# Performance work log

Measured on AMD Instinct MI355X. Metric: run time of the kernel, lower is better.

The kernel has to match this reference:

```python
import jax, jax.numpy as jnp
import numpy as np

ANCHORS = np.array([[4.63,1.97,1.74],[6.93,2.51,2.84],[6.37,2.85,3.19],[10.5,2.94,3.47],
                    [12.29,2.9,3.87],[0.5,2.53,0.98],[2.11,0.77,1.47],[1.7,0.6,1.28],
                    [0.73,0.67,1.77],[0.41,0.41,1.07]], dtype=np.float32)  # [10,3] nuScenes anchor sizes
BINS = 20          # anchor_size_bins
TEXT_DIM = 3 * BINS
NUM_PROPOSALS = 200
NMS_K = 3


def _vector_values():
    la = np.log(ANCHORS)
    return np.linspace(la.min() - 0.1, la.max() - 0.1, BINS).astype(np.float32)


def _anchor_vecs_normed():
    # soft_relu_bin_vectors: soft-bin log-anchors into BINS bins per dim, dim-major flatten
    vals = _vector_values()
    inc = vals[1] - vals[0]
    la = np.log(ANCHORS)                                      # [10,3]
    v = np.clip((la[:, :, None] - vals[None, None, :]) / inc, 0.0, 1.0)  # [10,3,BINS]
    v = v.reshape(10, TEXT_DIM)
    return (v / (1e-8 + np.linalg.norm(v, axis=1, keepdims=True))).astype(np.float32)


def conv2d(x, w, b=None):
    y = jax.lax.conv_general_dilated(x, w, (1, 1), 'SAME',
                                     dimension_numbers=('NCHW', 'OIHW', 'NCHW'))
    if b is not None:
        y = y + b[None, :, None, None]
    return y


def iou_sim_vec(a):
    # vectorized form of the triple-nested loop: prod over dims of min/max ratio
    mn = jnp.minimum(a[:, None, :], a[None, :, :])
    mx = jnp.maximum(a[:, None, :], a[None, :, :])
    return jnp.prod(mn / mx, axis=-1)                         # [10,10]


def setup_inputs() -> dict:
    key = jax.random.key(0)
    ks = jax.random.split(key, 8)
    B, Cin, hid, H, W = 2, 512, 128, 180, 180
    feats = jax.random.normal(ks[0], (B, Cin, H, W), jnp.float32)
    w_shared = jax.random.normal(ks[1], (hid, Cin, 3, 3), jnp.float32) * 0.02
    b_shared = jnp.zeros((hid,), jnp.float32)
    w_bb = jax.random.normal(ks[2], (hid, hid, 3, 3), jnp.float32) * 0.05
    gamma_bb = jnp.ones((hid,), jnp.float32)
    beta_bb = jnp.zeros((hid,), jnp.float32)
    w_hm = jax.random.normal(ks[3], (TEXT_DIM, hid, 3, 3), jnp.float32) * 0.05
    b_hm = jnp.zeros((TEXT_DIM,), jnp.float32)
    thr_scale = jnp.ones((1,), jnp.float32)                   # Threshold2d scale
    logit_scale = jnp.ones((1,), jnp.float32) * np.log(1.0 / 0.07)
    logit_bias = jnp.ones((1,), jnp.float32) * (-10.0)
    w_enc = jax.random.normal(ks[4], (hid, 3), jnp.float32) * 0.1  # Conv1d(3->hid, k=1)
    anchor_vecs = jnp.asarray(_anchor_vecs_normed())
    xs = jnp.arange(W, dtype=jnp.float32) + 0.5
    ys = jnp.arange(H, dtype=jnp.float32) + 0.5
    gy, gx = jnp.meshgrid(ys, xs, indexing='ij')
    bev_pos = jnp.stack([gx.reshape(-1), gy.reshape(-1)], axis=-1)  # [H*W, 2]
    return dict(feats=feats, w_shared=w_shared, b_shared=b_shared, w_bb=w_bb,
                gamma_bb=gamma_bb, beta_bb=beta_bb, w_hm=w_hm, b_hm=b_hm,
                thr_scale=thr_scale, logit_scale=logit_scale, logit_bias=logit_bias,
                w_enc=w_enc, anchor_vecs=anchor_vecs, bev_pos=bev_pos)


def reference(feats, w_shared, b_shared, w_bb, gamma_bb, beta_bb, w_hm, b_hm,
              thr_scale, logit_scale, logit_bias, w_enc, anchor_vecs, bev_pos):
    B, _, H, W = feats.shape
    # shared conv
    lidar_feat = conv2d(feats, w_shared, b_shared)            # [B,hid,H,W]
    # BasicBlock2D: conv + (inference) BN + ReLU
    x = conv2d(lidar_feat, w_bb)
    x = jax.nn.relu(x * gamma_bb[None, :, None, None] + beta_bb[None, :, None, None])
    # heatmap conv -> Threshold2d (sigmoid((x - thresholds) * scale))
    vec = conv2d(x, w_hm, b_hm)                               # [B,60,H,W]
    thresholds = jnp.asarray(np.tile(_vector_values(), 3))[None, :, None, None]
    vec = jax.nn.sigmoid((vec - thresholds) * thr_scale[0])
    # cosine sim vs normalized anchor bin-vectors -> per-class heatmap
    vecn = vec / (1e-8 + jnp.linalg.norm(vec, axis=1, keepdims=True))
    sim = jnp.einsum('bchw,kc->bkhw', vecn, anchor_vecs)      # [B,10,H,W]
    heatmap = jax.nn.sigmoid(logit_scale[0] * sim + logit_bias[0])
    # NMS: keep only local maxima within nms_kernel_size window
    local_max = jax.lax.reduce_window(heatmap, -jnp.inf, jax.lax.max,
                                      (1, 1, NMS_K, NMS_K), (1, 1, 1, 1), 'SAME')
    hm_nms = jnp.where(heatmap == local_max, heatmap, 0.0)
    # top-k proposals over classes x positions
    flat = hm_nms.reshape(B, -1)                              # [B, 10*H*W]
    top_scores, top_idx = jax.lax.top_k(flat, NUM_PROPOSALS)
    top_labels = top_idx // (H * W)                           # [B,P]
    top_pos = top_idx % (H * W)                               # [B,P]
    # gather proposal features, heatmap scores and bev positions
    hid = lidar_feat.shape[1]
    lidar_flat = lidar_feat.reshape(B, hid, H * W)
    idx_f = jnp.broadcast_to(top_pos[:, None, :], (B, hid, NUM_PROPOSALS))
    query_feat = jnp.take_along_axis(lidar_flat, idx_f, axis=2)  # [B,hid,P]
    hm_flat = heatmap.reshape(B, 10, H * W)
    idx_h = jnp.broadcast_to(top_pos[:, None, :], (B, 10, NUM_PROPOSALS))
    query_hm_score = jnp.take_along_axis(hm_flat, idx_h, axis=2)  # [B,10,P]
    query_pos = bev_pos[top_pos]                              # [B,P,2]
    # anchor value encoding (Conv1d(3->hid,k=1) on log-anchor sizes of top classes)
    top_anchor = jnp.log(jnp.asarray(ANCHORS))[top_labels]    # [B,P,3]
    query_feat = query_feat + jnp.einsum('cd,bpd->bcp', w_enc, top_anchor)
    sims = iou_sim_vec(jnp.asarray(ANCHORS))                  # [10,10] anchor IoU similarity
    return heatmap, top_scores, top_labels, query_feat, query_pos, query_hm_score, sims
```

## Files before the change

kernel.cpp:

```cpp
#include <hip/hip_runtime.h>
#include <math.h>


#define HW 180
#define NPIX 32400
#define NCLS 10
#define NPROP 200
#define HID 128
#define TDIM 60
#define NBIG (NCLS*NPIX)

#define TH_LO  (-0.9915981193)
#define TH_STEP (0.1789675812)

__constant__ float c_anchors[10][3] = {
  {4.63f,1.97f,1.74f},{6.93f,2.51f,2.84f},{6.37f,2.85f,3.19f},{10.5f,2.94f,3.47f},
  {12.29f,2.9f,3.87f},{0.5f,2.53f,0.98f},{2.11f,0.77f,1.47f},{1.7f,0.6f,1.28f},
  {0.73f,0.67f,1.77f},{0.41f,0.41f,1.07f}};

using f16x8 = _Float16 __attribute__((ext_vector_type(8)));
using f16x4 = _Float16 __attribute__((ext_vector_type(4)));
using f32x4 = float    __attribute__((ext_vector_type(4)));

#define GLD_LDS16(g, l) __builtin_amdgcn_global_load_lds( \
    (__attribute__((address_space(1))) void*)(g), \
    (__attribute__((address_space(3))) void*)(l), 16, 0, 0)

__device__ __forceinline__ void w_tr(const float* __restrict__ w, _Float16* __restrict__ dst,
                                     int CIN, int KS, int HALVES, int cout, int i) {
  int N = HALVES * KS * 36864;
  if (i >= N) return;
  int j = i & 7;
  int lane = (i >> 3) & 63;
  int mf = (i >> 9) & 3;
  int rest = i >> 11;
  int tsl = rest % 9; rest /= 9;
  int t = (tsl % 3) * 3 + (tsl / 3);
  int plane = rest & 1; rest >>= 1;
  int ks = rest % KS; int h = rest / KS;
  int co = h * 64 + mf * 16 + (lane & 15);
  int ch = ks * 32 + (lane >> 4) * 8 + j;
  float v = (co < cout) ? w[((size_t)co * CIN + ch) * 9 + t] : 0.f;
  _Float16 hi = (_Float16)v;
  dst[i] = plane ? (_Float16)(v - (float)hi) : hi;
}

__global__ __launch_bounds__(256)
void prep_kernel(const float* __restrict__ w_shared, const float* __restrict__ w_bb,
                 const float* __restrict__ w_hm, const float* __restrict__ feats,
                 _Float16* __restrict__ W1, _Float16* __restrict__ W2,
                 _Float16* __restrict__ W3, _Float16* __restrict__ X1,
                 float* __restrict__ out_sims, int* __restrict__ cnt) {
  int bid = blockIdx.x;
  const int tid = threadIdx.x;
  if (bid < 4608) { w_tr(w_shared, W1, 512, 16, 2, 128, bid * 256 + tid); return; }
  bid -= 4608;
  if (bid < 1152) { w_tr(w_bb, W2, 128, 4, 2, 128, bid * 256 + tid); return; }
  bid -= 1152;
  if (bid < 576)  { w_tr(w_hm, W3, 128, 4, 1, 60, bid * 256 + tid); return; }
  bid -= 576;
  if (bid < 4064) {
    int px = (bid % 127) * 256 + tid;
    int bks = bid / 127; int b = bks >> 4; int ks = bks & 15;
    if (px >= NPIX) return;
    const float* src = feats + ((size_t)(b * 512 + ks * 32)) * NPIX + px;
    float v[32];
#pragma unroll
    for (int c = 0; c < 32; ++c) v[c] = src[(size_t)c * NPIX];
    f16x8 hv[4], lv[4];
#pragma unroll
    for (int c = 0; c < 32; ++c) {
      _Float16 h = (_Float16)v[c];
      hv[c >> 3][c & 7] = h;
      lv[c >> 3][c & 7] = (_Float16)(v[c] - (float)h);
    }
    size_t ob = ((size_t)(b * 16 + ks) * NPIX + px) * 32;
#pragma unroll
    for (int i = 0; i < 4; ++i) {
      *(f16x8*)(X1 + ob + i * 8) = hv[i];
      *(f16x8*)(X1 + 33177600u + ob + i * 8) = lv[i];
    }
    return;
  }
  if (tid < 100) {
    int i = tid / 10, j = tid % 10;
    float r = 1.f;
#pragma unroll
    for (int d = 0; d < 3; ++d) {
      float ai = c_anchors[i][d], aj = c_anchors[j][d];
      r *= fminf(ai, aj) / fmaxf(ai, aj);
    }
    out_sims[tid] = r;
  }
  if (tid == 128) { cnt[0] = 0; cnt[1] = 0; }
}

template<int KS, int EPI>
__global__ __launch_bounds__(256, 2)
void conv_mfma(const _Float16* __restrict__ X, const _Float16* __restrict__ W,
               const float* __restrict__ p0, const float* __restrict__ p1,
               float* __restrict__ out0, _Float16* __restrict__ outX,
               const float* __restrict__ thr_scale, const float* __restrict__ logit_scale,
               const float* __restrict__ logit_bias, const float* __restrict__ anchor_vecs) {
  constexpr unsigned XPS = 2u * KS * NPIX * 32;
  constexpr bool DBUF = (EPI != 2);
  extern __shared__ _Float16 dlds[];
  _Float16* lds_x = dlds;
  _Float16* wA = dlds + 16128;
  _Float16* wB = dlds + 28416;
  float* lds_av = (float*)(dlds + 28416);

  const int x0 = blockIdx.x * 16;
  const int y0 = blockIdx.y * 12;
  const int b  = (EPI == 2) ? blockIdx.z : (blockIdx.z >> 1);
  const int h  = (EPI == 2) ? 0 : (blockIdx.z & 1);
  const int tid = threadIdx.x;
  const int wave = tid >> 6;
  const int lane = tid & 63;
  const int xl = lane & 15, kg = lane >> 4;

  {
    unsigned* p = (unsigned*)lds_x;
    for (int i = tid; i < 8064; i += 256) p[i] = 0u;
    if (EPI == 2)
      for (int i = tid; i < 600; i += 256) lds_av[i] = anchor_vecs[i];
  }

  unsigned offs[8]; unsigned okb = 0;
#pragma unroll
  for (int s = 0; s < 8; ++s) {
    int inst = wave + 4 * s;
    int c = inst * 64 + lane;
    bool valid = (c < 2016);
    int plane = (c >= 1008) ? 1 : 0;
    int cc = c - plane * 1008;
    int px = cc >> 2, q = cc & 3;
    int r = px / 18, xx = px - r * 18;
    int gy = y0 - 1 + r, gx = x0 - 1 + xx;
    bool ok = valid && ((unsigned)gy < 180u) && ((unsigned)gx < 180u);
    offs[s] = ok ? ((unsigned)((b * KS) * NPIX + gy * 180 + gx) * 32u + (unsigned)q * 8u
                    + (unsigned)plane * XPS) : 0u;
    okb |= (ok ? 1u : 0u) << s;
  }

  f32x4 acc[4][3];
#pragma unroll
  for (int mf = 0; mf < 4; ++mf)
#pragma unroll
    for (int f = 0; f < 3; ++f) acc[mf][f] = (f32x4){0.f, 0.f, 0.f, 0.f};

  auto COMPUTE = [&](int g, const _Float16* wbuf) {
    f16x8 bfh[5], bfl[5];
#pragma unroll
    for (int rr = 0; rr < 5; ++rr) {
      int lo = ((3 * wave + rr) * 18 + xl + g) * 32 + kg * 8;
      bfh[rr] = *(const f16x8*)(lds_x + lo);
      bfl[rr] = *(const f16x8*)(lds_x + 8064 + lo);
    }
#pragma unroll
    for (int ky = 0; ky < 3; ++ky) {
      const _Float16* wt = wbuf + ky * 2048 + lane * 8;
      f16x8 ah[4], al[4];
#pragma unroll
      for (int mf = 0; mf < 4; ++mf) {
        ah[mf] = *(const f16x8*)(wt + mf * 512);
        al[mf] = *(const f16x8*)(wt + 6144 + mf * 512);
      }
#pragma unroll
      for (int mf = 0; mf < 4; ++mf)
#pragma unroll
        for (int f = 0; f < 3; ++f) {
          acc[mf][f] = __builtin_amdgcn_mfma_f32_16x16x32_f16(ah[mf], bfh[f + ky], acc[mf][f], 0, 0, 0);
          acc[mf][f] = __builtin_amdgcn_mfma_f32_16x16x32_f16(ah[mf], bfl[f + ky], acc[mf][f], 0, 0, 0);
          acc[mf][f] = __builtin_amdgcn_mfma_f32_16x16x32_f16(al[mf], bfh[f + ky], acc[mf][f], 0, 0, 0);
        }
    }
  };
  auto WDMA = [&](const _Float16* gw, int g, _Float16* wbuf) {
#pragma unroll
    for (int s = 0; s < 6; ++s) {
      int c2 = wave + 4 * s;
      int pl = c2 / 12, idx = c2 - pl * 12;
      GLD_LDS16(gw + pl * 18432 + g * 6144 + idx * 512 + lane * 8,
                wbuf + pl * 6144 + idx * 512);
    }
  };
  auto XDMA = [&](unsigned kof) {
#pragma unroll
    for (int s = 0; s < 8; ++s) {
      if (okb & (1u << s))
        GLD_LDS16(X + (size_t)(offs[s] + kof), lds_x + (wave + 4 * s) * 512);
    }
  };

  const _Float16* gwb = W + (size_t)(h * KS) * 36864;
  for (int ks = 0; ks < KS; ++ks) {
    const unsigned kof = (unsigned)ks * (NPIX * 32u);
    const _Float16* gw = gwb + (size_t)ks * 36864;
    if (DBUF) {
      __syncthreads();
      XDMA(kof);
      WDMA(gw, 0, wA);
      __syncthreads();
      WDMA(gw, 1, wB);
      COMPUTE(0, wA);
      __syncthreads();
      WDMA(gw, 2, wA);
      COMPUTE(1, wB);
      __syncthreads();
      COMPUTE(2, wA);
    } else {
#pragma unroll
      for (int g = 0; g < 3; ++g) {
        __syncthreads();
        if (g == 0) XDMA(kof);
        WDMA(gw, g, wA);
        __syncthreads();
        COMPUTE(g, wA);
      }
    }
  }

  const int x = x0 + xl;
  if (EPI != 2) {
    if (x >= HW) return;
#pragma unroll
    for (int mf = 0; mf < 4; ++mf) {
      const int cobase = h * 64 + mf * 16 + kg * 4;
      f32x4 q0 = *(const f32x4*)(p0 + cobase);
      f32x4 q1 = (EPI == 1) ? *(const f32x4*)(p1 + cobase) : (f32x4){0.f,0.f,0.f,0.f};
#pragma unroll
      for (int f = 0; f < 3; ++f) {
        const int y = y0 + 3 * wave + f;
        const int kso = cobase >> 5, c32 = cobase & 31;
        size_t nidx = ((size_t)(b * 4 + kso) * NPIX + (size_t)y * 180 + x) * 32 + c32;
        if (EPI == 0) {
          f32x4 v;
          f16x4 h4, l4;
#pragma unroll
          for (int r = 0; r < 4; ++r) {
            float z = acc[mf][f][r] + q0[r];
            v[r] = z;
            _Float16 hh = (_Float16)z;
            h4[r] = hh;
            l4[r] = (_Float16)(z - (float)hh);
          }
          *(f32x4*)(out0 + nidx) = v;
          *(f16x4*)(outX + nidx) = h4;
          *(f16x4*)(outX + 8294400u + nidx) = l4;
        } else {
          f16x4 h4, l4;
#pragma unroll
          for (int r = 0; r < 4; ++r) {
            float z = fmaf(acc[mf][f][r], q0[r], q1[r]);
            z = fmaxf(z, 0.f);
            _Float16 hh = (_Float16)z;
            h4[r] = hh;
            l4[r] = (_Float16)(z - (float)hh);
          }
          *(f16x4*)(outX + nidx) = h4;
          *(f16x4*)(outX + 8294400u + nidx) = l4;
        }
      }
    }
  } else {
    const float s  = thr_scale[0];
    const float ls = logit_scale[0];
    const float lb = logit_bias[0];
    float bh4[4][4], th4[4][4];
    bool vmask[4];
#pragma unroll
    for (int mf = 0; mf < 4; ++mf) {
      const int cb = mf * 16 + kg * 4;
      vmask[mf] = (cb < TDIM);
#pragma unroll
      for (int r = 0; r < 4; ++r) {
        bh4[mf][r] = vmask[mf] ? p0[cb + r] : 0.f;
        th4[mf][r] = (float)(TH_LO + (double)((cb + r) % 20) * TH_STEP);
      }
    }
#pragma unroll
    for (int f = 0; f < 3; ++f) {
      const int y = y0 + 3 * wave + f;
      float v[4][4];
      float s2 = 0.f;
#pragma unroll
      for (int mf = 0; mf < 4; ++mf)
#pragma unroll
        for (int r = 0; r < 4; ++r) {
          float z = acc[mf][f][r] + bh4[mf][r];
          float t = (z - th4[mf][r]) * s;
          float vv = vmask[mf] ? 1.f / (1.f + expf(-t)) : 0.f;
          v[mf][r] = vv;
          s2 = fmaf(vv, vv, s2);
        }
      s2 += __shfl_xor(s2, 16);
      s2 += __shfl_xor(s2, 32);
      const float rs = 1.f / (1e-8f + sqrtf(s2));
      float hm[10];
#pragma unroll
      for (int k = 0; k < 10; ++k) {
        float d = 0.f;
#pragma unroll
        for (int mf = 0; mf < 4; ++mf) {
          const int cb = mf * 16 + kg * 4;
          f32x4 a = vmask[mf] ? *(const f32x4*)(lds_av + k * TDIM + cb)
                              : (f32x4){0.f, 0.f, 0.f, 0.f};
#pragma unroll
          for (int r = 0; r < 4; ++r) d = fmaf(v[mf][r], a[r], d);
        }
        d += __shfl_xor(d, 16);
        d += __shfl_xor(d, 32);
        hm[k] = 1.f / (1.f + expf(-fmaf(ls, d * rs, lb)));
      }
      if (x < HW) {
#pragma unroll
        for (int j = 0; j < 3; ++j) {
          int k = kg + 4 * j;
          if (k < NCLS)
            out0[((size_t)(b * NCLS + k) * HW + y) * HW + x] = hm[k];
        }
      }
    }
  }
}

__global__ __launch_bounds__(256)
void nms_kernel(const float* __restrict__ hm, float* __restrict__ ckey,
                int* __restrict__ cidx, int* __restrict__ cnt) {
  __shared__ int lcnt[2];
  __shared__ int lbase[2];
  const int tid = threadIdx.x;
  if (tid < 2) lcnt[tid] = 0;
  __syncthreads();

  int i = blockIdx.x * 256 + tid;
  bool surv = false; float v = 0.f; int bk = 0, p = 0;
  if (i < 2 * NBIG) {
    int x = i % HW; int y = (i / HW) % HW; int plane = i / NPIX;
    v = hm[i];
    float m = v;
#pragma unroll
    for (int dy = -1; dy <= 1; ++dy)
#pragma unroll
      for (int dx = -1; dx <= 1; ++dx) {
        int yy = y + dy, xx = x + dx;
        if ((unsigned)yy < (unsigned)HW && (unsigned)xx < (unsigned)HW)
          m = fmaxf(m, hm[((size_t)plane * NPIX) + yy * HW + xx]);
      }
    if (v == m) {
      surv = true;
      bk = i / NBIG;
      p = atomicAdd(&lcnt[bk], 1);
    }
  }
  __syncthreads();
  if (tid < 2 && lcnt[tid] > 0)
    lbase[tid] = atomicAdd(&cnt[tid], lcnt[tid]);
  __syncthreads();
  if (surv) {
    int slot = lbase[bk] + p;
    ckey[(size_t)bk * NBIG + slot] = v;
    cidx[(size_t)bk * NBIG + slot] = i - bk * NBIG;
  }
}

__global__ __launch_bounds__(1024)
void topk_kernel(const float* __restrict__ ckey, const int* __restrict__ cidx,
                 const int* __restrict__ cnt, const float* __restrict__ heatmap,
                 const float* __restrict__ bev_pos, float* __restrict__ out,
                 int* __restrict__ iws) {
  const int b = blockIdx.x;
  const int tid = threadIdx.x;
  const float* keys = ckey + (size_t)b * NBIG;
  const int* idxs = cidx + (size_t)b * NBIG;

  __shared__ unsigned hist[256];
  __shared__ unsigned sh_prefix;
  __shared__ int sh_want, sh_n;
  __shared__ int cntGT, cntTie;
  __shared__ unsigned gt_key[256], gt_idx[256];
  __shared__ unsigned tie_idx[2048];

  if (tid == 0) sh_n = cnt[b];
  __syncthreads();
  const int n = sh_n;

  unsigned prefix = 0; int want = NPROP;
  for (int shift = 24; shift >= 0; shift -= 8) {
    if (tid < 256) hist[tid] = 0u;
    __syncthreads();
    for (int i = tid; i < n; i += 1024) {
      unsigned k = __float_as_uint(keys[i]);
      bool match = (shift == 24) || ((k >> (shift + 8)) == (prefix >> (shift + 8)));
      if (match) atomicAdd(&hist[(k >> shift) & 255], 1u);
    }
    __syncthreads();
    if (tid == 0) {
      int cum = 0; int bsel = 0; sh_want = want;
      for (int bin = 255; bin >= 0; --bin) {
        cum += (int)hist[bin];
        if (cum >= want) { bsel = bin; sh_want = want - (cum - (int)hist[bin]); break; }
      }
      sh_prefix = prefix | ((unsigned)bsel << shift);
      cntGT = 0; cntTie = 0;
    }
    __syncthreads();
    prefix = sh_prefix; want = sh_want;
    __syncthreads();
  }
  const unsigned T = prefix;

  for (int i = tid; i < n; i += 1024) {
    unsigned k = __float_as_uint(keys[i]);
    if (k > T) {
      int p = atomicAdd(&cntGT, 1);
      if (p < 256) { gt_key[p] = k; gt_idx[p] = (unsigned)idxs[i]; }
    } else if (k == T) {
      int p = atomicAdd(&cntTie, 1);
      if (p < 2048) tie_idx[p] = (unsigned)idxs[i];
    }
  }
  __syncthreads();
  const int nGT = min(cntGT, 256);
  const int nTie = min(cntTie, 2048);

  for (int i = tid; i < 256; i += 1024)
    if (i >= nGT) { gt_key[i] = 0u; gt_idx[i] = 0xFFFFFFFFu; }
  for (int i = tid; i < 2048; i += 1024)
    if (i >= nTie) tie_idx[i] = 0xFFFFFFFFu;
  __syncthreads();

  for (int k2 = 2; k2 <= 256; k2 <<= 1) {
    for (int j = k2 >> 1; j > 0; j >>= 1) {
      for (int i = tid; i < 256; i += 1024) {
        int ixj = i ^ j;
        if (ixj > i) {
          unsigned ka = gt_key[i], kb = gt_key[ixj];
          unsigned ia = gt_idx[i], ib = gt_idx[ixj];
          bool firstA = (ka > kb) || (ka == kb && ia < ib);
          bool up = ((i & k2) == 0);
          if (up ? !firstA : firstA) {
            gt_key[i] = kb; gt_key[ixj] = ka;
            gt_idx[i] = ib; gt_idx[ixj] = ia;
          }
        }
      }
      __syncthreads();
    }
  }
  for (int k2 = 2; k2 <= 2048; k2 <<= 1) {
    for (int j = k2 >> 1; j > 0; j >>= 1) {
      for (int i = tid; i < 2048; i += 1024) {
        int ixj = i ^ j;
        if (ixj > i) {
          unsigned ia = tie_idx[i], ib = tie_idx[ixj];
          bool firstA = ia < ib;
          bool up = ((i & k2) == 0);
          if (up ? !firstA : firstA) { tie_idx[i] = ib; tie_idx[ixj] = ia; }
        }
      }
      __syncthreads();
    }
  }

  for (int r = tid; r < NPROP; r += 1024) {
    unsigned idx; float score;
    if (r < nGT) { idx = gt_idx[r]; score = __uint_as_float(gt_key[r]); }
    else         { idx = tie_idx[r - nGT]; score = __uint_as_float(T); }
    int label = (int)(idx / NPIX);
    int pos = (int)(idx - (unsigned)label * NPIX);
    out[648000 + b * NPROP + r] = score;
    out[648400 + b * NPROP + r] = (float)label;
    out[700000 + (b * NPROP + r) * 2 + 0] = bev_pos[pos * 2 + 0];
    out[700000 + (b * NPROP + r) * 2 + 1] = bev_pos[pos * 2 + 1];
#pragma unroll
    for (int k = 0; k < NCLS; ++k)
      out[700800 + (b * NCLS + k) * NPROP + r] = heatmap[(size_t)(b * NCLS + k) * NPIX + pos];
    iws[b * NPROP + r] = pos;
    iws[2 * NPROP + b * NPROP + r] = label;
  }
}

__global__ void gather_qf_kernel(const float* __restrict__ lidar, const float* __restrict__ w_enc,
                                 const int* __restrict__ iws, float* __restrict__ out_qf) {
  int p = blockIdx.x % NPROP;
  int b = blockIdx.x / NPROP;
  int c = threadIdx.x;
  int pos = iws[b * NPROP + p];
  int label = iws[2 * NPROP + b * NPROP + p];
  float la0 = logf(c_anchors[label][0]);
  float la1 = logf(c_anchors[label][1]);
  float la2 = logf(c_anchors[label][2]);
  float dot = w_enc[c * 3 + 0] * la0 + w_enc[c * 3 + 1] * la1 + w_enc[c * 3 + 2] * la2;
  float g = lidar[((size_t)(b * 4 + (c >> 5)) * NPIX + pos) * 32 + (c & 31)];
  out_qf[((size_t)b * HID + c) * NPROP + p] = g + dot;
}

extern "C" void kernel_launch(void* const* d_in, const int* in_sizes, int n_in,
                              void* d_out, int out_size, void* d_ws, size_t ws_size,
                              hipStream_t stream) {
  (void)in_sizes; (void)n_in; (void)out_size; (void)ws_size;
  const float* feats       = (const float*)d_in[0];
  const float* w_shared    = (const float*)d_in[1];
  const float* b_shared    = (const float*)d_in[2];
  const float* w_bb        = (const float*)d_in[3];
  const float* gamma_bb    = (const float*)d_in[4];
  const float* beta_bb     = (const float*)d_in[5];
  const float* w_hm        = (const float*)d_in[6];
  const float* b_hm        = (const float*)d_in[7];
  const float* thr_scale   = (const float*)d_in[8];
  const float* logit_scale = (const float*)d_in[9];
  const float* logit_bias  = (const float*)d_in[10];
  const float* w_enc       = (const float*)d_in[11];
  const float* anchor_vecs = (const float*)d_in[12];
  const float* bev_pos     = (const float*)d_in[13];
  float* out = (float*)d_out;

  float* ws = (float*)d_ws;
  size_t off = 0;
  _Float16* X1 = (_Float16*)(ws + off); off += 33177600;
  _Float16* X2 = (_Float16*)(ws + off); off += 8294400;
  float* lidarN = ws + off; off += 8294400;
  _Float16* X3 = (_Float16*)(ws + off); off += 8294400;
  _Float16* W1 = (_Float16*)(ws + off); off += 589824;
  _Float16* W2 = (_Float16*)(ws + off); off += 147456;
  _Float16* W3 = (_Float16*)(ws + off); off += 73728;
  float* ckey  = ws + off; off += (size_t)2 * NBIG;
  int*   cidx  = (int*)(ws + off); off += (size_t)2 * NBIG;
  int*   iws   = (int*)(ws + off); off += 800;
  int*   cnt   = (int*)(ws + off);

  prep_kernel<<<10401, 256, 0, stream>>>(w_shared, w_bb, w_hm, feats,
                                         W1, W2, W3, X1, out + 704800, cnt);

  const unsigned CONV_LDS = 81408;
  const unsigned HEAD_LDS = 59232;
  dim3 cgrid(12, 15, 4);
  conv_mfma<16,0><<<cgrid, 256, CONV_LDS, stream>>>(X1, W1, b_shared, nullptr, lidarN, X2,
                                                    nullptr, nullptr, nullptr, nullptr);
  conv_mfma<4, 1><<<cgrid, 256, CONV_LDS, stream>>>(X2, W2, gamma_bb, beta_bb, nullptr, X3,
                                                    nullptr, nullptr, nullptr, nullptr);
  dim3 hgrid(12, 15, 2);
  conv_mfma<4, 2><<<hgrid, 256, HEAD_LDS, stream>>>(X3, W3, b_hm, nullptr, out, nullptr,
                                                    thr_scale, logit_scale, logit_bias,
                                                    anchor_vecs);

  nms_kernel<<<(2*NBIG + 255)/256, 256, 0, stream>>>(out, ckey, cidx, cnt);
  topk_kernel<<<2, 1024, 0, stream>>>(ckey, cidx, cnt, out, bev_pos, out, iws);
  gather_qf_kernel<<<2*NPROP, 128, 0, stream>>>(lidarN, w_enc, iws, out + 648800);
}
```

Baseline: 519.8 us.

## Shrink conv LDS footprint by splitting weight planes and dropping double buffering

The conv kernel no longer double-buffers the hi/lo weight planes. It now loads the high weight plane into a single smaller LDS buffer, runs its MFMAs, then reloads the low plane into the same buffer for the remaining MFMA term. This cuts LDS per block and raises launch bounds to 3 waves-per-SIMD occupancy so more blocks can overlap. The cost is extra barriers per group and the loss of the overlap between weight DMA and compute.

```diff
diff --git a/kernel.cpp b/kernel.cpp
--- a/kernel.cpp
+++ b/kernel.cpp
@@ -96,19 +96,17 @@
 }
 
 template<int KS, int EPI>
-__global__ __launch_bounds__(256, 2)
+__global__ __launch_bounds__(256, 3)
 void conv_mfma(const _Float16* __restrict__ X, const _Float16* __restrict__ W,
                const float* __restrict__ p0, const float* __restrict__ p1,
                float* __restrict__ out0, _Float16* __restrict__ outX,
                const float* __restrict__ thr_scale, const float* __restrict__ logit_scale,
                const float* __restrict__ logit_bias, const float* __restrict__ anchor_vecs) {
   constexpr unsigned XPS = 2u * KS * NPIX * 32;
-  constexpr bool DBUF = (EPI != 2);
   extern __shared__ _Float16 dlds[];
   _Float16* lds_x = dlds;
-  _Float16* wA = dlds + 16128;
-  _Float16* wB = dlds + 28416;
-  float* lds_av = (float*)(dlds + 28416);
+  _Float16* lds_w = dlds + 16128;
+  float* lds_av = (float*)(dlds + 22272);
 
   const int x0 = blockIdx.x * 16;
   const int y0 = blockIdx.y * 12;
@@ -149,74 +147,67 @@
 #pragma unroll
     for (int f = 0; f < 3; ++f) acc[mf][f] = (f32x4){0.f, 0.f, 0.f, 0.f};
 
-  auto COMPUTE = [&](int g, const _Float16* wbuf) {
-    f16x8 bfh[5], bfl[5];
-#pragma unroll
-    for (int rr = 0; rr < 5; ++rr) {
-      int lo = ((3 * wave + rr) * 18 + xl + g) * 32 + kg * 8;
-      bfh[rr] = *(const f16x8*)(lds_x + lo);
-      bfl[rr] = *(const f16x8*)(lds_x + 8064 + lo);
-    }
-#pragma unroll
-    for (int ky = 0; ky < 3; ++ky) {
-      const _Float16* wt = wbuf + ky * 2048 + lane * 8;
-      f16x8 ah[4], al[4];
-#pragma unroll
-      for (int mf = 0; mf < 4; ++mf) {
-        ah[mf] = *(const f16x8*)(wt + mf * 512);
-        al[mf] = *(const f16x8*)(wt + 6144 + mf * 512);
-      }
-#pragma unroll
-      for (int mf = 0; mf < 4; ++mf)
-#pragma unroll
-        for (int f = 0; f < 3; ++f) {
-          acc[mf][f] = __builtin_amdgcn_mfma_f32_16x16x32_f16(ah[mf], bfh[f + ky], acc[mf][f], 0, 0, 0);
-          acc[mf][f] = __builtin_amdgcn_mfma_f32_16x16x32_f16(ah[mf], bfl[f + ky], acc[mf][f], 0, 0, 0);
-          acc[mf][f] = __builtin_amdgcn_mfma_f32_16x16x32_f16(al[mf], bfh[f + ky], acc[mf][f], 0, 0, 0);
-        }
-    }
-  };
-  auto WDMA = [&](const _Float16* gw, int g, _Float16* wbuf) {
-#pragma unroll
-    for (int s = 0; s < 6; ++s) {
-      int c2 = wave + 4 * s;
-      int pl = c2 / 12, idx = c2 - pl * 12;
-      GLD_LDS16(gw + pl * 18432 + g * 6144 + idx * 512 + lane * 8,
-                wbuf + pl * 6144 + idx * 512);
-    }
-  };
-  auto XDMA = [&](unsigned kof) {
-#pragma unroll
-    for (int s = 0; s < 8; ++s) {
-      if (okb & (1u << s))
-        GLD_LDS16(X + (size_t)(offs[s] + kof), lds_x + (wave + 4 * s) * 512);
-    }
-  };
-
   const _Float16* gwb = W + (size_t)(h * KS) * 36864;
+  f16x8 bfh[5], bfl[5];
+
   for (int ks = 0; ks < KS; ++ks) {
     const unsigned kof = (unsigned)ks * (NPIX * 32u);
     const _Float16* gw = gwb + (size_t)ks * 36864;
-    if (DBUF) {
+#pragma unroll
+    for (int g = 0; g < 3; ++g) {
       __syncthreads();
-      XDMA(kof);
-      WDMA(gw, 0, wA);
+      if (g == 0) {
+#pragma unroll
+        for (int s = 0; s < 8; ++s) {
+          if (okb & (1u << s))
+            GLD_LDS16(X + (size_t)(offs[s] + kof), lds_x + (wave + 4 * s) * 512);
+        }
+      }
+#pragma unroll
+      for (int s = 0; s < 3; ++s) {
+        int c2 = wave + 4 * s;
+        GLD_LDS16(gw + g * 6144 + c2 * 512 + lane * 8, lds_w + c2 * 512);
+      }
       __syncthreads();
-      WDMA(gw, 1, wB);
-      COMPUTE(0, wA);
+
+#pragma unroll
+      for (int rr = 0; rr < 5; ++rr) {
+        int lo = ((3 * wave + rr) * 18 + xl + g) * 32 + kg * 8;
+        bfh[rr] = *(const f16x8*)(lds_x + lo);
+        bfl[rr] = *(const f16x8*)(lds_x + 8064 + lo);
+      }
+#pragma unroll
+      for (int ky = 0; ky < 3; ++ky) {
+        const _Float16* wt = lds_w + ky * 2048 + lane * 8;
+        f16x8 ah[4];
+#pragma unroll
+        for (int mf = 0; mf < 4; ++mf) ah[mf] = *(const f16x8*)(wt + mf * 512);
+#pragma unroll
+        for (int mf = 0; mf < 4; ++mf)
+#pragma unroll
+          for (int f = 0; f < 3; ++f) {
+            acc[mf][f] = __builtin_amdgcn_mfma_f32_16x16x32_f16(ah[mf], bfh[f + ky], acc[mf][f], 0, 0, 0);
+            acc[mf][f] = __builtin_amdgcn_mfma_f32_16x16x32_f16(ah[mf], bfl[f + ky], acc[mf][f], 0, 0, 0);
+          }
+      }
       __syncthreads();
-      WDMA(gw, 2, wA);
-      COMPUTE(1, wB);
+#pragma unroll
+      for (int s = 0; s < 3; ++s) {
+        int c2 = wave + 4 * s;
+        GLD_LDS16(gw + 18432 + g * 6144 + c2 * 512 + lane * 8, lds_w + c2 * 512);
+      }
       __syncthreads();
-      COMPUTE(2, wA);
-    } else {
-#pragma unroll
-      for (int g = 0; g < 3; ++g) {
-        __syncthreads();
-        if (g == 0) XDMA(kof);
-        WDMA(gw, g, wA);
-        __syncthreads();
-        COMPUTE(g, wA);
+#pragma unroll
+      for (int ky = 0; ky < 3; ++ky) {
+        const _Float16* wt = lds_w + ky * 2048 + lane * 8;
+        f16x8 al[4];
+#pragma unroll
+        for (int mf = 0; mf < 4; ++mf) al[mf] = *(const f16x8*)(wt + mf * 512);
+#pragma unroll
+        for (int mf = 0; mf < 4; ++mf)
+#pragma unroll
+          for (int f = 0; f < 3; ++f)
+            acc[mf][f] = __builtin_amdgcn_mfma_f32_16x16x32_f16(al[mf], bfh[f + ky], acc[mf][f], 0, 0, 0);
       }
     }
   }
@@ -534,8 +525,8 @@
   prep_kernel<<<10401, 256, 0, stream>>>(w_shared, w_bb, w_hm, feats,
                                          W1, W2, W3, X1, out + 704800, cnt);
 
-  const unsigned CONV_LDS = 81408;
-  const unsigned HEAD_LDS = 59232;
+  const unsigned CONV_LDS = 44544;
+  const unsigned HEAD_LDS = 46944;
   dim3 cgrid(12, 15, 4);
   conv_mfma<16,0><<<cgrid, 256, CONV_LDS, stream>>>(X1, W1, b_shared, nullptr, lidarN, X2,
                                                     nullptr, nullptr, nullptr, nullptr);
```

Result: slower. 545.5 us (+4.9%).
